# Kernel tuning notes

Hardware: AMD Instinct MI355X
Metric: run time of the kernel (lower is better)

Reference implementation:

```python
import jax, jax.numpy as jnp
import numpy as np

N_NODES = 100000
N_EDGES = 1600000
D_IN = 128
D_HID = 128
D_OUT = 64
DROP_P = 0.5


def setup_inputs() -> dict:
    key = jax.random.key(0)
    ks = jax.random.split(key, 8)
    x = jax.random.normal(ks[0], (N_NODES, D_IN), dtype=jnp.float32)
    edge_index = jax.random.randint(ks[1], (2, N_EDGES), 0, N_NODES, dtype=jnp.int64)
    s = lambda fi, fo: 1.0 / np.sqrt(fi)
    W1_l = jax.random.uniform(ks[2], (D_IN, D_HID), jnp.float32, -s(D_IN, D_HID), s(D_IN, D_HID))
    W1_r = jax.random.uniform(ks[3], (D_IN, D_HID), jnp.float32, -s(D_IN, D_HID), s(D_IN, D_HID))
    b1 = jnp.zeros((D_HID,), jnp.float32)
    W2_l = jax.random.uniform(ks[4], (D_HID, D_OUT), jnp.float32, -s(D_HID, D_OUT), s(D_HID, D_OUT))
    W2_r = jax.random.uniform(ks[5], (D_HID, D_OUT), jnp.float32, -s(D_HID, D_OUT), s(D_HID, D_OUT))
    b2 = jnp.zeros((D_OUT,), jnp.float32)
    return {"x": x, "edge_index": edge_index, "W1_l": W1_l, "b1": b1, "W1_r": W1_r,
            "W2_l": W2_l, "b2": b2, "W2_r": W2_r}


def reference(x, edge_index, W1_l, b1, W1_r, W2_l, b2, W2_r):
    N = x.shape[0]
    src = edge_index[0]  # message source x_j
    dst = edge_index[1]  # aggregation target x_i
    # in-degree for mean aggregation (clamped to avoid div-by-zero)
    deg = jax.ops.segment_sum(jnp.ones((src.shape[0],), x.dtype), dst, num_segments=N)
    inv_deg = (1.0 / jnp.maximum(deg, 1.0))[:, None]  # [N,1]

    def sage(h, Wl, b, Wr):
        # mean over incoming neighbors, then lin_l(agg) + bias + lin_r(root)
        agg = jax.ops.segment_sum(h[src], dst, num_segments=N) * inv_deg  # [N,F]
        return agg @ Wl + b + h @ Wr

    h = jax.nn.relu(sage(x, W1_l, b1, W1_r))
    # dropout p=0.5 (training mode), deterministic key
    keep = jax.random.bernoulli(jax.random.key(42), 1.0 - DROP_P, h.shape)
    h = jnp.where(keep, h / (1.0 - DROP_P), 0.0)
    out = sage(h, W2_l, b2, W2_r)
    return jax.nn.log_softmax(out, axis=-1)
```

## Files before the change

kernel.cpp:

```cpp
#include <hip/hip_runtime.h>
#include <stdint.h>

#define D_FEAT 128
#define D_OUT  64
#define BSH 7
#define MAXB 1024
#define BCAP 4096

typedef __attribute__((ext_vector_type(8))) short short8;
typedef __attribute__((ext_vector_type(8))) ushort ushort8;
typedef __attribute__((ext_vector_type(4))) float f32x4;
typedef __attribute__((ext_vector_type(2))) float f32x2;

__device__ __forceinline__ ushort f2bf(float f) {
  uint32_t u = __float_as_uint(f);
  return (ushort)((u + 0x7FFFu + ((u >> 16) & 1u)) >> 16);
}
__device__ __forceinline__ float bf2f(ushort v) {
  return __uint_as_float((uint32_t)v << 16);
}
__device__ __forceinline__ void acc2(f32x2& a, uint32_t w) {
  f32x2 t;
  t.x = __uint_as_float(w << 16);
  t.y = __uint_as_float(w);
  a += t;
}
__device__ __forceinline__ void accq(f32x2& a, f32x2& b, uint32_t w) {
  a += __builtin_amdgcn_cvt_pk_f32_fp8(w, false);
  b += __builtin_amdgcn_cvt_pk_f32_fp8(w, true);
}

__device__ __forceinline__ void threefry2x32(uint32_t k0, uint32_t k1,
                                             uint32_t& x0, uint32_t& x1) {
  uint32_t k2 = k0 ^ k1 ^ 0x1BD11BDAu;
#define TF_ROT(r) { x0 += x1; x1 = (x1 << (r)) | (x1 >> (32 - (r))); x1 ^= x0; }
  x0 += k0; x1 += k1;
  TF_ROT(13) TF_ROT(15) TF_ROT(26) TF_ROT(6)
  x0 += k1; x1 += k2 + 1u;
  TF_ROT(17) TF_ROT(29) TF_ROT(16) TF_ROT(24)
  x0 += k2; x1 += k0 + 2u;
  TF_ROT(13) TF_ROT(15) TF_ROT(26) TF_ROT(6)
  x0 += k0; x1 += k1 + 3u;
  TF_ROT(17) TF_ROT(29) TF_ROT(16) TF_ROT(24)
  x0 += k1; x1 += k2 + 4u;
  TF_ROT(13) TF_ROT(15) TF_ROT(26) TF_ROT(6)
  x0 += k2; x1 += k0 + 5u;
#undef TF_ROT
}

__device__ __forceinline__ bool keep_bit(uint32_t i) {
  uint32_t t0 = 0u, t1 = i;
  threefry2x32(0u, 42u, t0, t1);
  return (((t0 ^ t1) >> 31) == 0u);
}

__global__ void detect_kernel(const uint32_t* __restrict__ ei, int* __restrict__ flag) {
  uint32_t v = ei[2 * threadIdx.x + 1];
  unsigned long long nz = __ballot(v != 0u);
  if (threadIdx.x == 0) flag[0] = (nz == 0ull) ? 1 : 0;
}

__device__ __forceinline__ int load_dst(const void* ei, int is64, long E, long e) {
  return is64 ? (int)((const long long*)ei)[E + e] : ((const int*)ei)[E + e];
}
__device__ __forceinline__ int load_src(const void* ei, int is64, long E, long e) {
  return is64 ? (int)((const long long*)ei)[e] : ((const int*)ei)[e];
}

__global__ __launch_bounds__(256) void convx_kernel(
    const float4* __restrict__ x, ushort* __restrict__ xb,
    uint8_t* __restrict__ xq, long n4) {
  long i = (long)blockIdx.x * blockDim.x + threadIdx.x;
  if (i >= n4) return;
  float4 v = x[i];
  ushort4 o = {f2bf(v.x), f2bf(v.y), f2bf(v.z), f2bf(v.w)};
  *(ushort4*)(xb + i * 4) = o;
  int p = 0;
  p = __builtin_amdgcn_cvt_pk_fp8_f32(v.x, v.y, p, false);
  p = __builtin_amdgcn_cvt_pk_fp8_f32(v.z, v.w, p, true);
  ((uint32_t*)xq)[i] = (uint32_t)p;
}

__global__ __launch_bounds__(256) void packw1_kernel(
    const float* __restrict__ Wl, const float* __restrict__ Wr,
    ushort* __restrict__ wt) {
  int idx = blockIdx.x * blockDim.x + threadIdx.x;
  if (idx >= 128 * 256) return;
  int j = idx >> 8, k = idx & 255;
  float v = (k < 128) ? Wl[k * 128 + j] : Wr[(k - 128) * 128 + j];
  wt[j * 256 + k] = f2bf(v);
}

__global__ __launch_bounds__(256) void packw2_kernel(
    const float* __restrict__ W, ushort* __restrict__ wt) {
  int idx = blockIdx.x * blockDim.x + threadIdx.x;
  if (idx >= 64 * 128) return;
  int j = idx >> 7, k = idx & 127;
  wt[j * 128 + k] = f2bf(W[k * 64 + j]);
}

__global__ void zrow_kernel(ushort* __restrict__ b0, uint8_t* __restrict__ q0,
                            int* __restrict__ bucketCur, int N) {
  if (threadIdx.x < 16)
    *(ushort8*)(b0 + (long)N * D_FEAT + threadIdx.x * 8) = (ushort8){0,0,0,0,0,0,0,0};
  else if (threadIdx.x < 24)
    *(uint4*)(q0 + (long)N * D_FEAT + (threadIdx.x - 16) * 16) = (uint4){0,0,0,0};
  int b = blockIdx.x * blockDim.x + threadIdx.x;
  if (b < MAXB) bucketCur[b] = b * BCAP;
}

__global__ __launch_bounds__(256) void bucket_scatter(
    const void* __restrict__ ei, const int* __restrict__ flag,
    int* __restrict__ bucketCur, uint32_t* __restrict__ packed,
    long E, int chunk, int nbuck) {
  __shared__ int cnt[MAXB];
  __shared__ int base[MAXB];
  __shared__ int cur[MAXB];
  const int is64 = flag[0];
  long beg = (long)blockIdx.x * chunk;
  long end = beg + chunk; if (end > E) end = E;
  for (int i = threadIdx.x; i < nbuck; i += 256) { cnt[i] = 0; cur[i] = 0; }
  __syncthreads();
  for (long e = beg + threadIdx.x; e < end; e += 256)
    atomicAdd(&cnt[load_dst(ei, is64, E, e) >> BSH], 1);
  __syncthreads();
  for (int i = threadIdx.x; i < nbuck; i += 256)
    base[i] = cnt[i] ? atomicAdd(&bucketCur[i], cnt[i]) : 0;
  __syncthreads();
  for (long e = beg + threadIdx.x; e < end; e += 256) {
    int dst = load_dst(ei, is64, E, e);
    int src = load_src(ei, is64, E, e);
    int b = dst >> BSH;
    int off = atomicAdd(&cur[b], 1);
    packed[base[b] + off] = ((uint32_t)src << BSH) | (uint32_t)(dst & ((1 << BSH) - 1));
  }
}

__global__ __launch_bounds__(256) void bucket_build(
    uint32_t* __restrict__ packed, const int* __restrict__ bucketCur,
    int* __restrict__ rowptr, int* __restrict__ rowend,
    float* __restrict__ invd, int N) {
  __shared__ uint32_t sp[BCAP];
  __shared__ int lcnt[1 << BSH];
  __shared__ int lbase[1 << BSH];
  __shared__ int lcur[1 << BSH];
  const int b = blockIdx.x;
  const int tid = threadIdx.x;
  const int beg = b * BCAP;
  const int cnt = bucketCur[b] - beg;
  for (int i = tid; i < cnt; i += 256) sp[i] = packed[beg + i];
  if (tid < 128) { lcnt[tid] = 0; lcur[tid] = 0; }
  __syncthreads();
  for (int i = tid; i < cnt; i += 256)
    atomicAdd(&lcnt[sp[i] & 127], 1);
  __syncthreads();
  if (tid < 128) lbase[tid] = lcnt[tid];
  __syncthreads();
  for (int off = 1; off < 128; off <<= 1) {
    int t = (tid >= off && tid < 128) ? lbase[tid - off] : 0;
    __syncthreads();
    if (tid < 128) lbase[tid] += t;
    __syncthreads();
  }
  if (tid < 128) {
    int excl = lbase[tid] - lcnt[tid];
    lbase[tid] = excl;
    int n = (b << BSH) + tid;
    if (n < N) {
      rowptr[n] = beg + excl;
      rowend[n] = beg + excl + lcnt[tid];
      int d = lcnt[tid];
      invd[n] = 1.0f / (float)(d > 1 ? d : 1);
    }
  }
  __syncthreads();
  for (int i = tid; i < cnt; i += 256) {
    uint32_t p = sp[i];
    int l = p & 127;
    int pos = beg + lbase[l] + atomicAdd(&lcur[l], 1);
    packed[pos] = p >> BSH;
  }
}

__global__ __launch_bounds__(256) void agg_kernel(
    const uint8_t* __restrict__ xq, const int* __restrict__ rowptr,
    const int* __restrict__ rowend, const int* __restrict__ col,
    const float* __restrict__ invd, ushort* __restrict__ aggb,
    unsigned long long* __restrict__ maskb, int N) {
  const int lane = threadIdx.x & 63;
  const int q  = lane >> 4;
  const int sl = lane & 15;
  const uint32_t slb = (uint32_t)sl * 8u;
  int n = (int)(((long)blockIdx.x * blockDim.x + threadIdx.x) >> 6);
  if (n >= N) return;

  if (maskb) {
    uint32_t base = (uint32_t)n * 128u;
    bool k0 = keep_bit(base + (uint32_t)lane);
    bool k1 = keep_bit(base + 64u + (uint32_t)lane);
    unsigned long long w0 = __ballot(k0);
    unsigned long long w1 = __ballot(k1);
    if (lane == 0) {
      maskb[2 * n]     = w0;
      maskb[2 * n + 1] = w1;
    }
  }

  const char* xc = (const char*)xq;
  const int beg = rowptr[n], end = rowend[n];
  const uint32_t zoff = ((uint32_t)N << 7) + slb;

  f32x2 acc[4];
#pragma unroll
  for (int i = 0; i < 4; i++) acc[i] = (f32x2){0.f, 0.f};

  for (int e = beg + q; e < end; e += 16) {
    int c0 = col[e], c1 = col[e + 4], c2 = col[e + 8], c3 = col[e + 12];
    uint32_t o0 = ((uint32_t)c0 << 7) + slb;
    uint32_t o1 = (e + 4  < end) ? (((uint32_t)c1 << 7) + slb) : zoff;
    uint32_t o2 = (e + 8  < end) ? (((uint32_t)c2 << 7) + slb) : zoff;
    uint32_t o3 = (e + 12 < end) ? (((uint32_t)c3 << 7) + slb) : zoff;
    uint2 a = *(const uint2*)(xc + o0);
    uint2 b = *(const uint2*)(xc + o1);
    uint2 c = *(const uint2*)(xc + o2);
    uint2 d = *(const uint2*)(xc + o3);
    accq(acc[0], acc[1], a.x); accq(acc[2], acc[3], a.y);
    accq(acc[0], acc[1], b.x); accq(acc[2], acc[3], b.y);
    accq(acc[0], acc[1], c.x); accq(acc[2], acc[3], c.y);
    accq(acc[0], acc[1], d.x); accq(acc[2], acc[3], d.y);
  }

#pragma unroll
  for (int i = 0; i < 4; i++) {
    acc[i].x += __shfl_xor(acc[i].x, 16);
    acc[i].y += __shfl_xor(acc[i].y, 16);
    acc[i].x += __shfl_xor(acc[i].x, 32);
    acc[i].y += __shfl_xor(acc[i].y, 32);
  }

  if (q == 0) {
    float sc = invd[n];
    ushort8 o;
#pragma unroll
    for (int i = 0; i < 4; i++) {
      o[2 * i]     = f2bf(acc[i].x * sc);
      o[2 * i + 1] = f2bf(acc[i].y * sc);
    }
    *(ushort8*)(aggb + (long)n * D_FEAT + sl * 8) = o;
  }
}

__global__ __launch_bounds__(256) void agg64_kernel(
    const ushort* __restrict__ featb, const int* __restrict__ rowptr,
    const int* __restrict__ rowend, const int* __restrict__ col,
    const float* __restrict__ invd, ushort* __restrict__ aggo, int N) {
  const int lane = threadIdx.x & 63;
  const int g  = lane >> 3;
  const int sl = lane & 7;
  const uint32_t slb = (uint32_t)sl * 16u;
  int n = (int)(((long)blockIdx.x * blockDim.x + threadIdx.x) >> 6);
  if (n >= N) return;

  const char* xc = (const char*)featb;
  const int beg = rowptr[n], end = rowend[n];
  const uint32_t zoff = ((uint32_t)N << 7) + slb;

  f32x2 acc[4];
#pragma unroll
  for (int i = 0; i < 4; i++) acc[i] = (f32x2){0.f, 0.f};

  for (int e = beg + g; e < end; e += 16) {
    int c0 = col[e], c1 = col[e + 8];
    uint32_t o0 = ((uint32_t)c0 << 7) + slb;
    uint32_t o1 = (e + 8 < end) ? (((uint32_t)c1 << 7) + slb) : zoff;
    uint4 a = *(const uint4*)(xc + o0);
    uint4 b = *(const uint4*)(xc + o1);
    acc2(acc[0], a.x); acc2(acc[1], a.y); acc2(acc[2], a.z); acc2(acc[3], a.w);
    acc2(acc[0], b.x); acc2(acc[1], b.y); acc2(acc[2], b.z); acc2(acc[3], b.w);
  }

#pragma unroll
  for (int i = 0; i < 4; i++) {
    acc[i].x += __shfl_xor(acc[i].x, 8);
    acc[i].y += __shfl_xor(acc[i].y, 8);
    acc[i].x += __shfl_xor(acc[i].x, 16);
    acc[i].y += __shfl_xor(acc[i].y, 16);
    acc[i].x += __shfl_xor(acc[i].x, 32);
    acc[i].y += __shfl_xor(acc[i].y, 32);
  }

  if (g == 0) {
    float sc = invd[n];
    ushort8 o;
#pragma unroll
    for (int i = 0; i < 4; i++) {
      o[2 * i]     = f2bf(acc[i].x * sc);
      o[2 * i + 1] = f2bf(acc[i].y * sc);
    }
    *(ushort8*)(aggo + (long)n * D_OUT + sl * 8) = o;
  }
}

__global__ __launch_bounds__(256) void layer1_kernel(
    const ushort* __restrict__ aggb, const ushort* __restrict__ xb,
    const ushort* __restrict__ w1t, const float* __restrict__ b1,
    const unsigned long long* __restrict__ maskb,
    ushort* __restrict__ h1d, int N) {
  __shared__ ushort w1s[128 * 256];
  const int tid = threadIdx.x;
  const int lane = tid & 63;
  const int wv = tid >> 6;
  const int r16 = lane & 15;
  const int kg = lane >> 4;

  {
    const uint32_t swz = ((uint32_t)(tid >> 5) & 7u) << 4;
#pragma unroll
    for (int i = 0; i < 16; i++) {
      uint32_t byte = (uint32_t)i * 4096u + (uint32_t)tid * 16u;
      uint4 v = *(const uint4*)((const char*)w1t + byte);
      *(uint4*)((char*)w1s + (byte ^ swz)) = v;
    }
  }
  __syncthreads();

  const int node_base = blockIdx.x * 128 + wv * 32;
  int ar0 = node_base + r16;       if (ar0 >= N) ar0 = N - 1;
  int ar1 = node_base + 16 + r16;  if (ar1 >= N) ar1 = N - 1;

  f32x4 acc0[8], acc1[8];
#pragma unroll
  for (int i = 0; i < 8; i++) {
    acc0[i] = (f32x4){0.f, 0.f, 0.f, 0.f};
    acc1[i] = (f32x4){0.f, 0.f, 0.f, 0.f};
  }

  const ushort* a0g = aggb + (long)ar0 * 128 + kg * 8;
  const ushort* a0x = xb   + (long)ar0 * 128 + kg * 8;
  const ushort* a1g = aggb + (long)ar1 * 128 + kg * 8;
  const ushort* a1x = xb   + (long)ar1 * 128 + kg * 8;
  const uint32_t rswz = ((uint32_t)(r16 & 7)) << 4;

#pragma unroll
  for (int s = 0; s < 8; s++) {
    short8 aT0 = (s < 4) ? *(const short8*)(a0g + s * 32)
                         : *(const short8*)(a0x + (s - 4) * 32);
    short8 aT1 = (s < 4) ? *(const short8*)(a1g + s * 32)
                         : *(const short8*)(a1x + (s - 4) * 32);
#pragma unroll
    for (int ct = 0; ct < 8; ct++) {
      uint32_t boff = ((uint32_t)(ct * 16 + r16) * 512u +
                       (uint32_t)s * 64u + (uint32_t)kg * 16u) ^ rswz;
      short8 b = *(const short8*)((const char*)w1s + boff);
      acc0[ct] = __builtin_amdgcn_mfma_f32_16x16x32_bf16(aT0, b, acc0[ct], 0, 0, 0);
      acc1[ct] = __builtin_amdgcn_mfma_f32_16x16x32_bf16(aT1, b, acc1[ct], 0, 0, 0);
    }
  }

  float bbv[8];
#pragma unroll
  for (int ct = 0; ct < 8; ct++) bbv[ct] = b1[ct * 16 + r16];

#pragma unroll
  for (int t = 0; t < 2; t++) {
    const f32x4* acc = t ? acc1 : acc0;
    int nb = node_base + t * 16;
#pragma unroll
    for (int r = 0; r < 4; r++) {
      int n = nb + kg * 4 + r;
      if (n < N) {
        unsigned long long m0 = maskb[2 * n];
        unsigned long long m1 = maskb[2 * n + 1];
#pragma unroll
        for (int ct = 0; ct < 8; ct++) {
          int j = ct * 16 + r16;
          float h = fmaxf(acc[ct][r] + bbv[ct], 0.f);
          unsigned long long w = (j & 64) ? m1 : m0;
          bool keep = (w >> (j & 63)) & 1ull;
          h1d[(long)n * 128 + j] = keep ? f2bf(2.0f * h) : (ushort)0;
        }
      }
    }
  }
}

__global__ __launch_bounds__(256) void layer2a_kernel(
    const ushort* __restrict__ h1d, const ushort* __restrict__ w2lt,
    const ushort* __restrict__ w2rt, const float* __restrict__ b2,
    ushort* __restrict__ y2, ushort* __restrict__ z, int N) {
  __shared__ ushort wsl[64 * 128];
  __shared__ ushort wsr[64 * 128];
  const int tid = threadIdx.x;
  const int lane = tid & 63;
  const int wv = tid >> 6;
  const int r16 = lane & 15;
  const int kg = lane >> 4;

  {
    const uint32_t swz = ((uint32_t)(tid >> 4) & 7u) << 4;
#pragma unroll
    for (int i = 0; i < 4; i++) {
      uint32_t byte = (uint32_t)i * 4096u + (uint32_t)tid * 16u;
      uint4 vl = *(const uint4*)((const char*)w2lt + byte);
      uint4 vr = *(const uint4*)((const char*)w2rt + byte);
      *(uint4*)((char*)wsl + (byte ^ swz)) = vl;
      *(uint4*)((char*)wsr + (byte ^ swz)) = vr;
    }
  }
  if (blockIdx.x == 0 && tid < 8)
    *(ushort8*)(y2 + (long)N * D_OUT + tid * 8) = (ushort8){0,0,0,0,0,0,0,0};
  __syncthreads();

  const int node_base = blockIdx.x * 128 + wv * 32;
  int ar0 = node_base + r16;       if (ar0 >= N) ar0 = N - 1;
  int ar1 = node_base + 16 + r16;  if (ar1 >= N) ar1 = N - 1;

  f32x4 accL0[4], accL1[4], accR0[4], accR1[4];
#pragma unroll
  for (int i = 0; i < 4; i++) {
    accL0[i] = (f32x4){0.f, 0.f, 0.f, 0.f};
    accL1[i] = (f32x4){0.f, 0.f, 0.f, 0.f};
    accR0[i] = (f32x4){0.f, 0.f, 0.f, 0.f};
    accR1[i] = (f32x4){0.f, 0.f, 0.f, 0.f};
  }

  const ushort* a0 = h1d + (long)ar0 * 128 + kg * 8;
  const ushort* a1 = h1d + (long)ar1 * 128 + kg * 8;
  const uint32_t rswz = ((uint32_t)(r16 & 7)) << 4;

#pragma unroll
  for (int s = 0; s < 4; s++) {
    short8 aT0 = *(const short8*)(a0 + s * 32);
    short8 aT1 = *(const short8*)(a1 + s * 32);
#pragma unroll
    for (int ct = 0; ct < 4; ct++) {
      uint32_t boff = ((uint32_t)(ct * 16 + r16) * 256u +
                       (uint32_t)s * 64u + (uint32_t)kg * 16u) ^ rswz;
      short8 bl = *(const short8*)((const char*)wsl + boff);
      short8 br = *(const short8*)((const char*)wsr + boff);
      accL0[ct] = __builtin_amdgcn_mfma_f32_16x16x32_bf16(aT0, bl, accL0[ct], 0, 0, 0);
      accL1[ct] = __builtin_amdgcn_mfma_f32_16x16x32_bf16(aT1, bl, accL1[ct], 0, 0, 0);
      accR0[ct] = __builtin_amdgcn_mfma_f32_16x16x32_bf16(aT0, br, accR0[ct], 0, 0, 0);
      accR1[ct] = __builtin_amdgcn_mfma_f32_16x16x32_bf16(aT1, br, accR1[ct], 0, 0, 0);
    }
  }

  float bb[4];
#pragma unroll
  for (int ct = 0; ct < 4; ct++) bb[ct] = b2[ct * 16 + r16];

#pragma unroll
  for (int t = 0; t < 2; t++) {
    const f32x4* aL = t ? accL1 : accL0;
    const f32x4* aR = t ? accR1 : accR0;
    int nb = node_base + t * 16;
#pragma unroll
    for (int r = 0; r < 4; r++) {
      int n = nb + kg * 4 + r;
      if (n < N) {
#pragma unroll
        for (int ct = 0; ct < 4; ct++) {
          y2[(long)n * D_OUT + ct * 16 + r16] = f2bf(aL[ct][r]);
          z [(long)n * D_OUT + ct * 16 + r16] = f2bf(aR[ct][r] + bb[ct]);
        }
      }
    }
  }
}

__global__ __launch_bounds__(256) void softmax_kernel(
    const ushort* __restrict__ z, const ushort* __restrict__ aggy,
    float* __restrict__ out, int N) {
  const int lane = threadIdx.x & 63;
  int n = (int)(((long)blockIdx.x * blockDim.x + threadIdx.x) >> 6);
  if (n >= N) return;
  float v = bf2f(z[(long)n * D_OUT + lane]) + bf2f(aggy[(long)n * D_OUT + lane]);
  float m = v;
#pragma unroll
  for (int off = 1; off < 64; off <<= 1) m = fmaxf(m, __shfl_xor(m, off));
  float e = expf(v - m);
  float s = e;
#pragma unroll
  for (int off = 1; off < 64; off <<= 1) s += __shfl_xor(s, off);
  out[(long)n * D_OUT + lane] = v - m - logf(s);
}

extern "C" void kernel_launch(void* const* d_in, const int* in_sizes, int n_in,
                              void* d_out, int out_size, void* d_ws, size_t ws_size,
                              hipStream_t stream) {
  const float* x   = (const float*)d_in[0];
  const void*  ei  = d_in[1];
  const float* W1l = (const float*)d_in[2];
  const float* b1  = (const float*)d_in[3];
  const float* W1r = (const float*)d_in[4];
  const float* W2l = (const float*)d_in[5];
  const float* b2  = (const float*)d_in[6];
  const float* W2r = (const float*)d_in[7];
  float* out = (float*)d_out;

  const int  N  = in_sizes[0] / D_FEAT;
  const long E  = (long)in_sizes[1] / 2;
  const long NF = (long)N * D_FEAT;
  const int  nbuck = (N + (1 << BSH) - 1) >> BSH;

  char* ws = (char*)d_ws;
  size_t off = 0;
  auto alloc = [&](size_t bytes) -> void* {
    void* p = ws + off;
    off = (off + bytes + 255) & ~(size_t)255;
    return p;
  };
  int*      bucketCur = (int*)alloc(sizeof(int) * MAXB);
  int*      rowptr    = (int*)alloc(sizeof(int) * N);
  int*      rowend    = (int*)alloc(sizeof(int) * N);
  uint32_t* packed    = (uint32_t*)alloc(sizeof(uint32_t) * ((size_t)nbuck * BCAP + 16));
  float*    invd      = (float*)alloc(sizeof(float) * N);
  ushort*   xb        = (ushort*)alloc(sizeof(ushort) * (NF + D_FEAT));
  uint8_t*  xq        = (uint8_t*)alloc(sizeof(uint8_t) * (NF + D_FEAT));
  ushort*   aggb      = (ushort*)alloc(sizeof(ushort) * (NF + 256));
  ushort*   h1d       = (ushort*)alloc(sizeof(ushort) * NF);
  ushort*   w1t       = (ushort*)alloc(sizeof(ushort) * 128 * 256);
  ushort*   w2lt      = (ushort*)alloc(sizeof(ushort) * 64 * 128);
  ushort*   w2rt      = (ushort*)alloc(sizeof(ushort) * 64 * 128);
  unsigned long long* maskb = (unsigned long long*)alloc(sizeof(unsigned long long) * 2 * N);
  int*      flag      = (int*)alloc(sizeof(int));

  int* col = (int*)packed;
  ushort* y2   = aggb;
  ushort* aggy = aggb + ((size_t)NF / 2 + 128);
  ushort* z    = (ushort*)xq;

  const int NBLK = 512;
  const int chunkE = (int)((E + NBLK - 1) / NBLK);

  detect_kernel<<<1, 64, 0, stream>>>((const uint32_t*)ei, flag);
  convx_kernel<<<(int)((NF / 4 + 255) / 256), 256, 0, stream>>>((const float4*)x, xb, xq, NF / 4);
  zrow_kernel<<<MAXB / 256, 256, 0, stream>>>(xb, xq, bucketCur, N);
  packw1_kernel<<<128, 256, 0, stream>>>(W1l, W1r, w1t);
  packw2_kernel<<<32, 256, 0, stream>>>(W2l, w2lt);
  packw2_kernel<<<32, 256, 0, stream>>>(W2r, w2rt);

  bucket_scatter<<<NBLK, 256, 0, stream>>>(ei, flag, bucketCur, packed, E, chunkE, nbuck);
  bucket_build<<<nbuck, 256, 0, stream>>>(packed, bucketCur, rowptr, rowend, invd, N);

  const int aggBlocks = (int)(((long)N * 64 + 255) / 256);
  const int gemmBlocks = (N + 127) / 128;

  agg_kernel<<<aggBlocks, 256, 0, stream>>>(xq, rowptr, rowend, col, invd, aggb, maskb, N);
  layer1_kernel<<<gemmBlocks, 256, 0, stream>>>(aggb, xb, w1t, b1, maskb, h1d, N);

  layer2a_kernel<<<gemmBlocks, 256, 0, stream>>>(h1d, w2lt, w2rt, b2, y2, z, N);
  agg64_kernel<<<aggBlocks, 256, 0, stream>>>(y2, rowptr, rowend, col, invd, aggy, N);
  softmax_kernel<<<aggBlocks, 256, 0, stream>>>(z, aggy, out, N);
}
```

Measured before the change: 214.9 us.

## Fuse layer1 and layer2 GEMMs via shared memory and fold softmax into agg64

Merges the layer-1 GEMM with the layer-2 dense transforms, so the dropout-masked hidden activations stay in LDS (padded rows) instead of going through a global h1d buffer. It also merges the log-softmax into the final aggregation kernel, which removes the aggy buffer and two kernel launches. The shared-memory footprint is reused across phases and needs an extra barrier, and the softmax now runs only on one 8-lane group per node.

```diff
diff --git a/kernel.cpp b/kernel.cpp
--- a/kernel.cpp
+++ b/kernel.cpp
@@ -6,6 +6,7 @@
 #define BSH 7
 #define MAXB 1024
 #define BCAP 4096
+#define H1P  136
 
 typedef __attribute__((ext_vector_type(8))) short short8;
 typedef __attribute__((ext_vector_type(8))) ushort ushort8;
@@ -100,11 +101,14 @@
 }
 
 __global__ void zrow_kernel(ushort* __restrict__ b0, uint8_t* __restrict__ q0,
-                            int* __restrict__ bucketCur, int N) {
+                            ushort* __restrict__ y2, int* __restrict__ bucketCur,
+                            int N) {
   if (threadIdx.x < 16)
     *(ushort8*)(b0 + (long)N * D_FEAT + threadIdx.x * 8) = (ushort8){0,0,0,0,0,0,0,0};
   else if (threadIdx.x < 24)
     *(uint4*)(q0 + (long)N * D_FEAT + (threadIdx.x - 16) * 16) = (uint4){0,0,0,0};
+  else if (threadIdx.x < 32)
+    *(ushort8*)(y2 + (long)N * D_OUT + (threadIdx.x - 24) * 8) = (ushort8){0,0,0,0,0,0,0,0};
   int b = blockIdx.x * blockDim.x + threadIdx.x;
   if (b < MAXB) bucketCur[b] = b * BCAP;
 }
@@ -250,10 +254,167 @@
   }
 }
 
+__global__ __launch_bounds__(256) void fused12_kernel(
+    const ushort* __restrict__ aggb, const ushort* __restrict__ xb,
+    const ushort* __restrict__ w1t, const float* __restrict__ b1,
+    const unsigned long long* __restrict__ maskb,
+    const ushort* __restrict__ w2lt, const ushort* __restrict__ w2rt,
+    const float* __restrict__ b2,
+    ushort* __restrict__ y2, ushort* __restrict__ z, int N) {
+  __shared__ __align__(16) ushort smem[33792];
+  ushort* w1s = smem;
+  ushort* h1s = smem;
+  ushort* wsl = smem + 17408;
+  ushort* wsr = smem + 25600;
+
+  const int tid = threadIdx.x;
+  const int lane = tid & 63;
+  const int wv = tid >> 6;
+  const int r16 = lane & 15;
+  const int kg = lane >> 4;
+
+  {
+    const uint32_t swz = ((uint32_t)(tid >> 5) & 7u) << 4;
+#pragma unroll
+    for (int i = 0; i < 16; i++) {
+      uint32_t byte = (uint32_t)i * 4096u + (uint32_t)tid * 16u;
+      uint4 v = *(const uint4*)((const char*)w1t + byte);
+      *(uint4*)((char*)w1s + (byte ^ swz)) = v;
+    }
+  }
+  __syncthreads();
+
+  const int node_base = blockIdx.x * 128 + wv * 32;
+  int ar0 = node_base + r16;       if (ar0 >= N) ar0 = N - 1;
+  int ar1 = node_base + 16 + r16;  if (ar1 >= N) ar1 = N - 1;
+
+  f32x4 acc0[8], acc1[8];
+#pragma unroll
+  for (int i = 0; i < 8; i++) {
+    acc0[i] = (f32x4){0.f, 0.f, 0.f, 0.f};
+    acc1[i] = (f32x4){0.f, 0.f, 0.f, 0.f};
+  }
+
+  {
+    const ushort* a0g = aggb + (long)ar0 * 128 + kg * 8;
+    const ushort* a0x = xb   + (long)ar0 * 128 + kg * 8;
+    const ushort* a1g = aggb + (long)ar1 * 128 + kg * 8;
+    const ushort* a1x = xb   + (long)ar1 * 128 + kg * 8;
+    const uint32_t rswz = ((uint32_t)(r16 & 7)) << 4;
+#pragma unroll
+    for (int s = 0; s < 8; s++) {
+      short8 aT0 = (s < 4) ? *(const short8*)(a0g + s * 32)
+                           : *(const short8*)(a0x + (s - 4) * 32);
+      short8 aT1 = (s < 4) ? *(const short8*)(a1g + s * 32)
+                           : *(const short8*)(a1x + (s - 4) * 32);
+#pragma unroll
+      for (int ct = 0; ct < 8; ct++) {
+        uint32_t boff = ((uint32_t)(ct * 16 + r16) * 512u +
+                         (uint32_t)s * 64u + (uint32_t)kg * 16u) ^ rswz;
+        short8 b = *(const short8*)((const char*)w1s + boff);
+        acc0[ct] = __builtin_amdgcn_mfma_f32_16x16x32_bf16(aT0, b, acc0[ct], 0, 0, 0);
+        acc1[ct] = __builtin_amdgcn_mfma_f32_16x16x32_bf16(aT1, b, acc1[ct], 0, 0, 0);
+      }
+    }
+  }
+  __syncthreads();
+
+  {
+    const uint32_t swz = ((uint32_t)(tid >> 4) & 7u) << 4;
+#pragma unroll
+    for (int i = 0; i < 4; i++) {
+      uint32_t byte = (uint32_t)i * 4096u + (uint32_t)tid * 16u;
+      uint4 vl = *(const uint4*)((const char*)w2lt + byte);
+      uint4 vr = *(const uint4*)((const char*)w2rt + byte);
+      *(uint4*)((char*)wsl + (byte ^ swz)) = vl;
+      *(uint4*)((char*)wsr + (byte ^ swz)) = vr;
+    }
+  }
+
+  {
+    float bbv[8];
+#pragma unroll
+    for (int ct = 0; ct < 8; ct++) bbv[ct] = b1[ct * 16 + r16];
+#pragma unroll
+    for (int t = 0; t < 2; t++) {
+      const f32x4* acc = t ? acc1 : acc0;
+#pragma unroll
+      for (int r = 0; r < 4; r++) {
+        int row_l = wv * 32 + t * 16 + kg * 4 + r;
+        int n = blockIdx.x * 128 + row_l;
+        int mi = (n < N) ? n : (N - 1);
+        unsigned long long m0 = maskb[2 * mi];
+        unsigned long long m1 = maskb[2 * mi + 1];
+        ushort* dst = h1s + row_l * H1P + r16;
+#pragma unroll
+        for (int ct = 0; ct < 8; ct++) {
+          int j = ct * 16 + r16;
+          float h = fmaxf(acc[ct][r] + bbv[ct], 0.f);
+          unsigned long long w = (j & 64) ? m1 : m0;
+          bool keep = (w >> (j & 63)) & 1ull;
+          dst[ct * 16] = keep ? f2bf(2.0f * h) : (ushort)0;
+        }
+      }
+    }
+  }
+  __syncthreads();
+
+  f32x4 aL[2][4], aR[2][4];
+#pragma unroll
+  for (int t = 0; t < 2; t++)
+#pragma unroll
+    for (int i = 0; i < 4; i++) {
+      aL[t][i] = (f32x4){0.f, 0.f, 0.f, 0.f};
+      aR[t][i] = (f32x4){0.f, 0.f, 0.f, 0.f};
+    }
+
+  {
+    const uint32_t rswz = ((uint32_t)(r16 & 7)) << 4;
+#pragma unroll
+    for (int s = 0; s < 4; s++) {
+#pragma unroll
+      for (int t = 0; t < 2; t++) {
+        const ushort* ap = h1s + (wv * 32 + t * 16 + r16) * H1P + s * 32 + kg * 8;
+        short8 a = *(const short8*)ap;
+#pragma unroll
+        for (int ct = 0; ct < 4; ct++) {
+          uint32_t boff = ((uint32_t)(ct * 16 + r16) * 256u +
+                           (uint32_t)s * 64u + (uint32_t)kg * 16u) ^ rswz;
+          short8 bl = *(const short8*)((const char*)wsl + boff);
+          short8 br = *(const short8*)((const char*)wsr + boff);
+          aL[t][ct] = __builtin_amdgcn_mfma_f32_16x16x32_bf16(a, bl, aL[t][ct], 0, 0, 0);
+          aR[t][ct] = __builtin_amdgcn_mfma_f32_16x16x32_bf16(a, br, aR[t][ct], 0, 0, 0);
+        }
+      }
+    }
+  }
+
+  float bb[4];
+#pragma unroll
+  for (int ct = 0; ct < 4; ct++) bb[ct] = b2[ct * 16 + r16];
+
+#pragma unroll
+  for (int t = 0; t < 2; t++) {
+    int nb = node_base + t * 16;
+#pragma unroll
+    for (int r = 0; r < 4; r++) {
+      int n = nb + kg * 4 + r;
+      if (n < N) {
+#pragma unroll
+        for (int ct = 0; ct < 4; ct++) {
+          y2[(long)n * D_OUT + ct * 16 + r16] = f2bf(aL[t][ct][r]);
+          z [(long)n * D_OUT + ct * 16 + r16] = f2bf(aR[t][ct][r] + bb[ct]);
+        }
+      }
+    }
+  }
+}
+
 __global__ __launch_bounds__(256) void agg64_kernel(
-    const ushort* __restrict__ featb, const int* __restrict__ rowptr,
-    const int* __restrict__ rowend, const int* __restrict__ col,
-    const float* __restrict__ invd, ushort* __restrict__ aggo, int N) {
+    const ushort* __restrict__ y2, const ushort* __restrict__ z,
+    const int* __restrict__ rowptr, const int* __restrict__ rowend,
+    const int* __restrict__ col, const float* __restrict__ invd,
+    float* __restrict__ out, int N) {
   const int lane = threadIdx.x & 63;
   const int g  = lane >> 3;
   const int sl = lane & 7;
@@ -261,7 +422,7 @@
   int n = (int)(((long)blockIdx.x * blockDim.x + threadIdx.x) >> 6);
   if (n >= N) return;
 
-  const char* xc = (const char*)featb;
+  const char* xc = (const char*)y2;
   const int beg = rowptr[n], end = rowend[n];
   const uint32_t zoff = ((uint32_t)N << 7) + slb;
 
@@ -291,198 +452,32 @@
 
   if (g == 0) {
     float sc = invd[n];
-    ushort8 o;
+    ushort8 zr = *(const ushort8*)(z + (long)n * D_OUT + sl * 8);
+    float v[8];
 #pragma unroll
     for (int i = 0; i < 4; i++) {
-      o[2 * i]     = f2bf(acc[i].x * sc);
-      o[2 * i + 1] = f2bf(acc[i].y * sc);
-    }
-    *(ushort8*)(aggo + (long)n * D_OUT + sl * 8) = o;
-  }
-}
-
-__global__ __launch_bounds__(256) void layer1_kernel(
-    const ushort* __restrict__ aggb, const ushort* __restrict__ xb,
-    const ushort* __restrict__ w1t, const float* __restrict__ b1,
-    const unsigned long long* __restrict__ maskb,
-    ushort* __restrict__ h1d, int N) {
-  __shared__ ushort w1s[128 * 256];
-  const int tid = threadIdx.x;
-  const int lane = tid & 63;
-  const int wv = tid >> 6;
-  const int r16 = lane & 15;
-  const int kg = lane >> 4;
-
-  {
-    const uint32_t swz = ((uint32_t)(tid >> 5) & 7u) << 4;
-#pragma unroll
-    for (int i = 0; i < 16; i++) {
-      uint32_t byte = (uint32_t)i * 4096u + (uint32_t)tid * 16u;
-      uint4 v = *(const uint4*)((const char*)w1t + byte);
-      *(uint4*)((char*)w1s + (byte ^ swz)) = v;
-    }
-  }
-  __syncthreads();
-
-  const int node_base = blockIdx.x * 128 + wv * 32;
-  int ar0 = node_base + r16;       if (ar0 >= N) ar0 = N - 1;
-  int ar1 = node_base + 16 + r16;  if (ar1 >= N) ar1 = N - 1;
-
-  f32x4 acc0[8], acc1[8];
-#pragma unroll
-  for (int i = 0; i < 8; i++) {
-    acc0[i] = (f32x4){0.f, 0.f, 0.f, 0.f};
-    acc1[i] = (f32x4){0.f, 0.f, 0.f, 0.f};
-  }
-
-  const ushort* a0g = aggb + (long)ar0 * 128 + kg * 8;
-  const ushort* a0x = xb   + (long)ar0 * 128 + kg * 8;
-  const ushort* a1g = aggb + (long)ar1 * 128 + kg * 8;
-  const ushort* a1x = xb   + (long)ar1 * 128 + kg * 8;
-  const uint32_t rswz = ((uint32_t)(r16 & 7)) << 4;
-
-#pragma unroll
-  for (int s = 0; s < 8; s++) {
-    short8 aT0 = (s < 4) ? *(const short8*)(a0g + s * 32)
-                         : *(const short8*)(a0x + (s - 4) * 32);
-    short8 aT1 = (s < 4) ? *(const short8*)(a1g + s * 32)
-                         : *(const short8*)(a1x + (s - 4) * 32);
-#pragma unroll
-    for (int ct = 0; ct < 8; ct++) {
-      uint32_t boff = ((uint32_t)(ct * 16 + r16) * 512u +
-                       (uint32_t)s * 64u + (uint32_t)kg * 16u) ^ rswz;
-      short8 b = *(const short8*)((const char*)w1s + boff);
-      acc0[ct] = __builtin_amdgcn_mfma_f32_16x16x32_bf16(aT0, b, acc0[ct], 0, 0, 0);
-      acc1[ct] = __builtin_amdgcn_mfma_f32_16x16x32_bf16(aT1, b, acc1[ct], 0, 0, 0);
-    }
-  }
-
-  float bbv[8];
-#pragma unroll
-  for (int ct = 0; ct < 8; ct++) bbv[ct] = b1[ct * 16 + r16];
-
-#pragma unroll
-  for (int t = 0; t < 2; t++) {
-    const f32x4* acc = t ? acc1 : acc0;
-    int nb = node_base + t * 16;
-#pragma unroll
-    for (int r = 0; r < 4; r++) {
-      int n = nb + kg * 4 + r;
-      if (n < N) {
-        unsigned long long m0 = maskb[2 * n];
-        unsigned long long m1 = maskb[2 * n + 1];
-#pragma unroll
-        for (int ct = 0; ct < 8; ct++) {
-          int j = ct * 16 + r16;
-          float h = fmaxf(acc[ct][r] + bbv[ct], 0.f);
-          unsigned long long w = (j & 64) ? m1 : m0;
-          bool keep = (w >> (j & 63)) & 1ull;
-          h1d[(long)n * 128 + j] = keep ? f2bf(2.0f * h) : (ushort)0;
-        }
-      }
-    }
-  }
-}
-
-__global__ __launch_bounds__(256) void layer2a_kernel(
-    const ushort* __restrict__ h1d, const ushort* __restrict__ w2lt,
-    const ushort* __restrict__ w2rt, const float* __restrict__ b2,
-    ushort* __restrict__ y2, ushort* __restrict__ z, int N) {
-  __shared__ ushort wsl[64 * 128];
-  __shared__ ushort wsr[64 * 128];
-  const int tid = threadIdx.x;
-  const int lane = tid & 63;
-  const int wv = tid >> 6;
-  const int r16 = lane & 15;
-  const int kg = lane >> 4;
-
-  {
-    const uint32_t swz = ((uint32_t)(tid >> 4) & 7u) << 4;
-#pragma unroll
-    for (int i = 0; i < 4; i++) {
-      uint32_t byte = (uint32_t)i * 4096u + (uint32_t)tid * 16u;
-      uint4 vl = *(const uint4*)((const char*)w2lt + byte);
-      uint4 vr = *(const uint4*)((const char*)w2rt + byte);
-      *(uint4*)((char*)wsl + (byte ^ swz)) = vl;
-      *(uint4*)((char*)wsr + (byte ^ swz)) = vr;
-    }
-  }
-  if (blockIdx.x == 0 && tid < 8)
-    *(ushort8*)(y2 + (long)N * D_OUT + tid * 8) = (ushort8){0,0,0,0,0,0,0,0};
-  __syncthreads();
-
-  const int node_base = blockIdx.x * 128 + wv * 32;
-  int ar0 = node_base + r16;       if (ar0 >= N) ar0 = N - 1;
-  int ar1 = node_base + 16 + r16;  if (ar1 >= N) ar1 = N - 1;
-
-  f32x4 accL0[4], accL1[4], accR0[4], accR1[4];
-#pragma unroll
-  for (int i = 0; i < 4; i++) {
-    accL0[i] = (f32x4){0.f, 0.f, 0.f, 0.f};
-    accL1[i] = (f32x4){0.f, 0.f, 0.f, 0.f};
-    accR0[i] = (f32x4){0.f, 0.f, 0.f, 0.f};
-    accR1[i] = (f32x4){0.f, 0.f, 0.f, 0.f};
-  }
-
-  const ushort* a0 = h1d + (long)ar0 * 128 + kg * 8;
-  const ushort* a1 = h1d + (long)ar1 * 128 + kg * 8;
-  const uint32_t rswz = ((uint32_t)(r16 & 7)) << 4;
-
-#pragma unroll
-  for (int s = 0; s < 4; s++) {
-    short8 aT0 = *(const short8*)(a0 + s * 32);
-    short8 aT1 = *(const short8*)(a1 + s * 32);
-#pragma unroll
-    for (int ct = 0; ct < 4; ct++) {
-      uint32_t boff = ((uint32_t)(ct * 16 + r16) * 256u +
-                       (uint32_t)s * 64u + (uint32_t)kg * 16u) ^ rswz;
-      short8 bl = *(const short8*)((const char*)wsl + boff);
-      short8 br = *(const short8*)((const char*)wsr + boff);
-      accL0[ct] = __builtin_amdgcn_mfma_f32_16x16x32_bf16(aT0, bl, accL0[ct], 0, 0, 0);
-      accL1[ct] = __builtin_amdgcn_mfma_f32_16x16x32_bf16(aT1, bl, accL1[ct], 0, 0, 0);
-      accR0[ct] = __builtin_amdgcn_mfma_f32_16x16x32_bf16(aT0, br, accR0[ct], 0, 0, 0);
-      accR1[ct] = __builtin_amdgcn_mfma_f32_16x16x32_bf16(aT1, br, accR1[ct], 0, 0, 0);
-    }
-  }
-
-  float bb[4];
-#pragma unroll
-  for (int ct = 0; ct < 4; ct++) bb[ct] = b2[ct * 16 + r16];
-
-#pragma unroll
-  for (int t = 0; t < 2; t++) {
-    const f32x4* aL = t ? accL1 : accL0;
-    const f32x4* aR = t ? accR1 : accR0;
-    int nb = node_base + t * 16;
-#pragma unroll
-    for (int r = 0; r < 4; r++) {
-      int n = nb + kg * 4 + r;
-      if (n < N) {
-#pragma unroll
-        for (int ct = 0; ct < 4; ct++) {
-          y2[(long)n * D_OUT + ct * 16 + r16] = f2bf(aL[ct][r]);
-          z [(long)n * D_OUT + ct * 16 + r16] = f2bf(aR[ct][r] + bb[ct]);
-        }
-      }
-    }
-  }
-}
-
-__global__ __launch_bounds__(256) void softmax_kernel(
-    const ushort* __restrict__ z, const ushort* __restrict__ aggy,
-    float* __restrict__ out, int N) {
-  const int lane = threadIdx.x & 63;
-  int n = (int)(((long)blockIdx.x * blockDim.x + threadIdx.x) >> 6);
-  if (n >= N) return;
-  float v = bf2f(z[(long)n * D_OUT + lane]) + bf2f(aggy[(long)n * D_OUT + lane]);
-  float m = v;
-#pragma unroll
-  for (int off = 1; off < 64; off <<= 1) m = fmaxf(m, __shfl_xor(m, off));
-  float e = expf(v - m);
-  float s = e;
-#pragma unroll
-  for (int off = 1; off < 64; off <<= 1) s += __shfl_xor(s, off);
-  out[(long)n * D_OUT + lane] = v - m - logf(s);
+      v[2 * i]     = acc[i].x * sc + bf2f(zr[2 * i]);
+      v[2 * i + 1] = acc[i].y * sc + bf2f(zr[2 * i + 1]);
+    }
+    float m = v[0];
+#pragma unroll
+    for (int j = 1; j < 8; j++) m = fmaxf(m, v[j]);
+    m = fmaxf(m, __shfl_xor(m, 1));
+    m = fmaxf(m, __shfl_xor(m, 2));
+    m = fmaxf(m, __shfl_xor(m, 4));
+    float s = 0.f;
+#pragma unroll
+    for (int j = 0; j < 8; j++) s += expf(v[j] - m);
+    s += __shfl_xor(s, 1);
+    s += __shfl_xor(s, 2);
+    s += __shfl_xor(s, 4);
+    float ls = m + logf(s);
+    float4 o0 = {v[0] - ls, v[1] - ls, v[2] - ls, v[3] - ls};
+    float4 o1 = {v[4] - ls, v[5] - ls, v[6] - ls, v[7] - ls};
+    float* op = out + (long)n * D_OUT + sl * 8;
+    *(float4*)op = o0;
+    *(float4*)(op + 4) = o1;
+  }
 }
 
 extern "C" void kernel_launch(void* const* d_in, const int* in_sizes, int n_in,
@@ -517,8 +512,8 @@
   float*    invd      = (float*)alloc(sizeof(float) * N);
   ushort*   xb        = (ushort*)alloc(sizeof(ushort) * (NF + D_FEAT));
   uint8_t*  xq        = (uint8_t*)alloc(sizeof(uint8_t) * (NF + D_FEAT));
-  ushort*   aggb      = (ushort*)alloc(sizeof(ushort) * (NF + 256));
-  ushort*   h1d       = (ushort*)alloc(sizeof(ushort) * NF);
+  ushort*   aggb      = (ushort*)alloc(sizeof(ushort) * NF);
+  ushort*   yz        = (ushort*)alloc(sizeof(ushort) * (NF + 512));
   ushort*   w1t       = (ushort*)alloc(sizeof(ushort) * 128 * 256);
   ushort*   w2lt      = (ushort*)alloc(sizeof(ushort) * 64 * 128);
   ushort*   w2rt      = (ushort*)alloc(sizeof(ushort) * 64 * 128);
@@ -526,16 +521,15 @@
   int*      flag      = (int*)alloc(sizeof(int));
 
   int* col = (int*)packed;
-  ushort* y2   = aggb;
-  ushort* aggy = aggb + ((size_t)NF / 2 + 128);
-  ushort* z    = (ushort*)xq;
+  ushort* y2 = yz;
+  ushort* z  = yz + ((size_t)N * D_OUT + 256);
 
   const int NBLK = 512;
   const int chunkE = (int)((E + NBLK - 1) / NBLK);
 
   detect_kernel<<<1, 64, 0, stream>>>((const uint32_t*)ei, flag);
   convx_kernel<<<(int)((NF / 4 + 255) / 256), 256, 0, stream>>>((const float4*)x, xb, xq, NF / 4);
-  zrow_kernel<<<MAXB / 256, 256, 0, stream>>>(xb, xq, bucketCur, N);
+  zrow_kernel<<<MAXB / 256, 256, 0, stream>>>(xb, xq, y2, bucketCur, N);
   packw1_kernel<<<128, 256, 0, stream>>>(W1l, W1r, w1t);
   packw2_kernel<<<32, 256, 0, stream>>>(W2l, w2lt);
   packw2_kernel<<<32, 256, 0, stream>>>(W2r, w2rt);
@@ -547,9 +541,7 @@
   const int gemmBlocks = (N + 127) / 128;
 
   agg_kernel<<<aggBlocks, 256, 0, stream>>>(xq, rowptr, rowend, col, invd, aggb, maskb, N);
-  layer1_kernel<<<gemmBlocks, 256, 0, stream>>>(aggb, xb, w1t, b1, maskb, h1d, N);
-
-  layer2a_kernel<<<gemmBlocks, 256, 0, stream>>>(h1d, w2lt, w2rt, b2, y2, z, N);
-  agg64_kernel<<<aggBlocks, 256, 0, stream>>>(y2, rowptr, rowend, col, invd, aggy, N);
-  softmax_kernel<<<aggBlocks, 256, 0, stream>>>(z, aggy, out, N);
-}
+  fused12_kernel<<<gemmBlocks, 256, 0, stream>>>(aggb, xb, w1t, b1, maskb,
+                                                 w2lt, w2rt, b2, y2, z, N);
+  agg64_kernel<<<aggBlocks, 256, 0, stream>>>(y2, z, rowptr, rowend, col, invd, out, N);
+}
```

New measurement: 199.9 us. 1.08x faster.
